# Optimization experiments

Measured on AMD Instinct MI355X. Metric: run time of the kernel, lower is better.

The kernel has to match this reference:

```python
import jax, jax.numpy as jnp
import numpy as np

NUM_CLASSES = 19
EPS_MEAN = 1e-6   # torch: denominator eps in per-class mean
EPS_COS = 1e-8    # torch CosineSimilarity default eps


def _nearest_resize_labels(target, H, W):
    # torch nn.Upsample(mode='nearest'): in_idx = floor(out_idx * in / out)
    th, tw = target.shape[1], target.shape[2]
    ih = (jnp.arange(H) * th) // H
    iw = (jnp.arange(W) * tw) // W
    return target[:, ih][:, :, iw]  # [B,H,W]


def _class_centers(feat, lab):
    # feat: [B,C,H,W]; lab: [B,H,W] int. Single-pass segment mean by class,
    # then scatter means back to pixels whose label is in [0, NUM_CLASSES).
    B, C, H, W = feat.shape
    f = feat.reshape(B, C, H * W)                 # [B,C,N]
    l = lab.reshape(B, H * W)                      # [B,N]
    onehot = jax.nn.one_hot(l, NUM_CLASSES, dtype=feat.dtype)  # [B,N,K]; out-of-range -> all-zero row
    sums = jnp.einsum('bcn,bnk->bck', f, onehot)   # per-class channel sums
    counts = onehot.sum(axis=1)                    # [B,K]
    means = sums / (counts[:, None, :] + EPS_MEAN) # [B,C,K]
    gathered = jnp.einsum('bck,bnk->bcn', means, onehot)  # mean at each valid pixel, 0 elsewhere
    valid = (l >= 0) & (l < NUM_CLASSES)           # [B,N]
    center = jnp.where(valid[:, None, :], gathered, f)
    return center.reshape(B, C, H, W)


def _cosine_dim1(a, b):
    # torch CosineSimilarity(dim=1): dot / (max(||a||,eps) * max(||b||,eps))
    num = (a * b).sum(axis=1)
    na = jnp.sqrt((a * a).sum(axis=1))
    nb = jnp.sqrt((b * b).sum(axis=1))
    return num / (jnp.maximum(na, EPS_COS) * jnp.maximum(nb, EPS_COS))


def setup_inputs() -> dict:
    key = jax.random.key(0)
    k1, k2, k3 = jax.random.split(key, 3)
    B, C, H, W = 8, 512, 64, 64
    preds_S = jax.random.normal(k1, (B, C, H, W), dtype=jnp.float32)
    preds_T = jax.random.normal(k2, (B, C, H, W), dtype=jnp.float32)
    target = jax.random.randint(k3, (B, 512, 512), 0, NUM_CLASSES, dtype=jnp.int64)
    return {"preds_S": preds_S, "preds_T": preds_T, "target": target}


def reference(preds_S, preds_T, target):
    H, W = preds_S.shape[2], preds_S.shape[3]
    lab = _nearest_resize_labels(target, H, W)     # [B,H,W]
    center_S = _class_centers(preds_S, lab)
    center_T = _class_centers(preds_T, lab)
    pcsim_S = _cosine_dim1(preds_S, center_S)      # [B,H,W]
    pcsim_T = _cosine_dim1(preds_T, center_T)
    return jnp.mean((pcsim_S - pcsim_T) ** 2)
```

## Files before the change

### kernel.cpp

```cpp
#include <hip/hip_runtime.h>

#define NCLS   19
#define NB     8
#define NC     512
#define NHW    4096
#define EPSM   1e-6f
#define EPSC   1e-8f

#define OFF_LABELS   0u
#define OFF_COUNTS   131072u
#define OFF_SUMS_S   132096u
#define OFF_SUMS_T   443392u
#define OFF_NORM_S   754688u
#define OFF_NORM_T   755712u
#define OFF_PART     756736u

template<int CTRL>
__device__ __forceinline__ float dpp_add(float x) {
    int y = __builtin_amdgcn_update_dpp(0, __float_as_int(x), CTRL, 0xf, 0xf, false);
    return x + __int_as_float(y);
}
__device__ __forceinline__ float wave64_sum(float x) {
    x = dpp_add<0x111>(x);
    x = dpp_add<0x112>(x);
    x = dpp_add<0x114>(x);
    x = dpp_add<0x118>(x);
    x = dpp_add<0x142>(x);
    x = dpp_add<0x143>(x);
    return x;
}

__global__ __launch_bounds__(256) void k_labels(const int* __restrict__ target,
                                                int* __restrict__ labels,
                                                float* __restrict__ counts) {
    __shared__ int hist[NCLS];
    const int b = blockIdx.x;
    const int t = threadIdx.x;
    if (t < NCLS) hist[t] = 0;
    __syncthreads();
    const int* tb = target + (size_t)b * 512 * 512;
    #pragma unroll
    for (int i = 0; i < 16; ++i) {
        int n = t + i * 256;
        int y = n >> 6, x = n & 63;
        int l = tb[(y * 8) * 512 + x * 8];
        labels[b * NHW + n] = l;
        if (l >= 0 && l < NCLS) atomicAdd(&hist[l], 1);
    }
    __syncthreads();
    if (t < NCLS) counts[b * NCLS + t] = (float)hist[t];
}

__global__ __launch_bounds__(256, 2) void k_sums(const float* __restrict__ fS,
                                                 const float* __restrict__ fT,
                                                 const int* __restrict__ labels,
                                                 float* __restrict__ sumsS,
                                                 float* __restrict__ sumsT) {
    const int t = threadIdx.x;
    const int lane = t & 63;
    const int u = (blockIdx.x << 2) + (t >> 6);
    const int b = u >> 8;
    const int c0 = (u & 255) << 1;
    const size_t base = ((size_t)(b * NC) + c0) * NHW;
    const float4* pS0 = (const float4*)(fS + base);
    const float4* pS1 = (const float4*)(fS + base + NHW);
    const float4* pT0 = (const float4*)(fT + base);
    const float4* pT1 = (const float4*)(fT + base + NHW);
    const int4* lab4 = (const int4*)(labels + b * NHW);

    float aS0[NCLS], aS1[NCLS], aT0[NCLS], aT1[NCLS];
    #pragma unroll
    for (int k = 0; k < NCLS; ++k) { aS0[k] = aS1[k] = aT0[k] = aT1[k] = 0.f; }

    #pragma unroll 2
    for (int i = 0; i < 16; ++i) {
        const int idx = lane + (i << 6);
        const float4 vS0 = pS0[idx];
        const float4 vS1 = pS1[idx];
        const float4 vT0 = pT0[idx];
        const float4 vT1 = pT1[idx];
        const int4 l4 = lab4[idx];
        #pragma unroll
        for (int k = 0; k < NCLS; ++k) {
            const float m0 = (l4.x == k) ? 1.f : 0.f;
            const float m1 = (l4.y == k) ? 1.f : 0.f;
            const float m2 = (l4.z == k) ? 1.f : 0.f;
            const float m3 = (l4.w == k) ? 1.f : 0.f;
            aS0[k] += m0 * vS0.x + m1 * vS0.y + m2 * vS0.z + m3 * vS0.w;
            aS1[k] += m0 * vS1.x + m1 * vS1.y + m2 * vS1.z + m3 * vS1.w;
            aT0[k] += m0 * vT0.x + m1 * vT0.y + m2 * vT0.z + m3 * vT0.w;
            aT1[k] += m0 * vT1.x + m1 * vT1.y + m2 * vT1.z + m3 * vT1.w;
        }
    }
    #pragma unroll
    for (int k = 0; k < NCLS; ++k) {
        aS0[k] = wave64_sum(aS0[k]);
        aS1[k] = wave64_sum(aS1[k]);
        aT0[k] = wave64_sum(aT0[k]);
        aT1[k] = wave64_sum(aT1[k]);
    }
    if (lane == 63) {
        #pragma unroll
        for (int k = 0; k < NCLS; ++k) {
            float2* dS = (float2*)(sumsS + ((size_t)(b * NCLS + k)) * NC + c0);
            float2* dT = (float2*)(sumsT + ((size_t)(b * NCLS + k)) * NC + c0);
            *dS = make_float2(aS0[k], aS1[k]);
            *dT = make_float2(aT0[k], aT1[k]);
        }
    }
}

__global__ __launch_bounds__(64) void k_means(float* __restrict__ sumsS,
                                              float* __restrict__ sumsT,
                                              const float* __restrict__ counts,
                                              float* __restrict__ normS,
                                              float* __restrict__ normT) {
    const int bk = blockIdx.x;
    const int t = threadIdx.x;
    const float inv = 1.f / (counts[bk] + EPSM);
    float* rS = sumsS + (size_t)bk * NC;
    float* rT = sumsT + (size_t)bk * NC;
    float aS = 0.f, aT = 0.f;
    #pragma unroll
    for (int i = 0; i < NC / 64; ++i) {
        float mS = rS[t + i * 64] * inv; rS[t + i * 64] = mS; aS += mS * mS;
        float mT = rT[t + i * 64] * inv; rT[t + i * 64] = mT; aT += mT * mT;
    }
    aS = wave64_sum(aS);
    aT = wave64_sum(aT);
    if (t == 63) { normS[bk] = sqrtf(aS); normT[bk] = sqrtf(aT); }
}

#define CCH 64
__global__ __launch_bounds__(256) void k_dots(const float* __restrict__ fS,
                                              const float* __restrict__ fT,
                                              const float* __restrict__ meansS,
                                              const float* __restrict__ meansT,
                                              const int* __restrict__ labels,
                                              float* __restrict__ part) {
    __shared__ float mS[NCLS * 65];
    __shared__ float mT[NCLS * 65];
    const int blk = blockIdx.x;
    const int chunk = blk & 7;
    const int tile  = (blk >> 3) & 15;
    const int b     = blk >> 7;
    const int t = threadIdx.x;
    const int c0 = chunk * CCH;
    const int n = tile * 256 + t;

    for (int i = t; i < NCLS * CCH; i += 256) {
        const int k = i >> 6, j = i & 63;
        mS[k * 65 + j] = meansS[((size_t)(b * NCLS + k)) * NC + c0 + j];
        mT[k * 65 + j] = meansT[((size_t)(b * NCLS + k)) * NC + c0 + j];
    }
    __syncthreads();

    const int l = labels[b * NHW + n];
    const int lc = (l >= 0 && l < NCLS) ? l : 0;
    const float* pS = fS + ((size_t)(b * NC + c0)) * NHW + n;
    const float* pT = fT + ((size_t)(b * NC + c0)) * NHW + n;
    float dS = 0.f, nS = 0.f, dT = 0.f, nT = 0.f;
    #pragma unroll 8
    for (int ci = 0; ci < CCH; ++ci) {
        const float vS = pS[(size_t)ci * NHW];
        const float vT = pT[(size_t)ci * NHW];
        const float ms = mS[lc * 65 + ci];
        const float mt = mT[lc * 65 + ci];
        dS += vS * ms; nS += vS * vS;
        dT += vT * mt; nT += vT * vT;
    }
    const int p = b * NHW + n;
    part[((size_t)(0 * 8 + chunk)) * (NB * NHW) + p] = dS;
    part[((size_t)(1 * 8 + chunk)) * (NB * NHW) + p] = nS;
    part[((size_t)(2 * 8 + chunk)) * (NB * NHW) + p] = dT;
    part[((size_t)(3 * 8 + chunk)) * (NB * NHW) + p] = nT;
}

__global__ __launch_bounds__(256) void k_final(const float* __restrict__ part,
                                               const int* __restrict__ labels,
                                               const float* __restrict__ normS,
                                               const float* __restrict__ normT,
                                               float* __restrict__ out) {
    __shared__ float red[4];
    const int p = blockIdx.x * 256 + threadIdx.x;
    const int b = p >> 12;
    float dS = 0.f, nS = 0.f, dT = 0.f, nT = 0.f;
    #pragma unroll
    for (int ch = 0; ch < 8; ++ch) {
        dS += part[((size_t)(0 * 8 + ch)) * (NB * NHW) + p];
        nS += part[((size_t)(1 * 8 + ch)) * (NB * NHW) + p];
        dT += part[((size_t)(2 * 8 + ch)) * (NB * NHW) + p];
        nT += part[((size_t)(3 * 8 + ch)) * (NB * NHW) + p];
    }
    const int l = labels[p];
    float val = 0.f;
    if (l >= 0 && l < NCLS) {
        float cS = dS / (fmaxf(sqrtf(nS), EPSC) * fmaxf(normS[b * NCLS + l], EPSC));
        float cT = dT / (fmaxf(sqrtf(nT), EPSC) * fmaxf(normT[b * NCLS + l], EPSC));
        float d = cS - cT;
        val = d * d;
    }
    val = wave64_sum(val);
    if ((threadIdx.x & 63) == 63) red[threadIdx.x >> 6] = val;
    __syncthreads();
    if (threadIdx.x == 0)
        atomicAdd(out, (red[0] + red[1] + red[2] + red[3]) * (1.f / (NB * NHW)));
}

extern "C" void kernel_launch(void* const* d_in, const int* in_sizes, int n_in,
                              void* d_out, int out_size, void* d_ws, size_t ws_size,
                              hipStream_t stream) {
    (void)in_sizes; (void)n_in; (void)out_size; (void)ws_size;
    const float* fS     = (const float*)d_in[0];
    const float* fT     = (const float*)d_in[1];
    const int*   target = (const int*)d_in[2];

    char* ws = (char*)d_ws;
    int*   labels = (int*)  (ws + OFF_LABELS);
    float* counts = (float*)(ws + OFF_COUNTS);
    float* sumsS  = (float*)(ws + OFF_SUMS_S);
    float* sumsT  = (float*)(ws + OFF_SUMS_T);
    float* normS  = (float*)(ws + OFF_NORM_S);
    float* normT  = (float*)(ws + OFF_NORM_T);
    float* part   = (float*)(ws + OFF_PART);

    hipMemsetAsync(d_out, 0, sizeof(float), stream);

    k_labels<<<NB, 256, 0, stream>>>(target, labels, counts);
    k_sums  <<<NB * NC / 8, 256, 0, stream>>>(fS, fT, labels, sumsS, sumsT);
    k_means <<<NB * NCLS, 64, 0, stream>>>(sumsS, sumsT, counts, normS, normT);
    k_dots  <<<NB * 16 * 8, 256, 0, stream>>>(fS, fT, sumsS, sumsT, labels, part);
    k_final <<<NB * NHW / 256, 256, 0, stream>>>(part, labels, normS, normT,
                                                 (float*)d_out);
}
```

Measured before the change: 207.8 us.

## Replace masked per-class register accumulation with LDS atomic scatter-add in k_sums

```diff
diff --git a/kernel.cpp b/kernel.cpp
--- a/kernel.cpp
+++ b/kernel.cpp
@@ -6,6 +6,7 @@
 #define NHW    4096
 #define EPSM   1e-6f
 #define EPSC   1e-8f
+#define GCH    2
 
 #define OFF_LABELS   0u
 #define OFF_COUNTS   131072u
@@ -51,62 +52,51 @@
     if (t < NCLS) counts[b * NCLS + t] = (float)hist[t];
 }
 
-__global__ __launch_bounds__(256, 2) void k_sums(const float* __restrict__ fS,
-                                                 const float* __restrict__ fT,
-                                                 const int* __restrict__ labels,
-                                                 float* __restrict__ sumsS,
-                                                 float* __restrict__ sumsT) {
-    const int t = threadIdx.x;
-    const int lane = t & 63;
-    const int u = (blockIdx.x << 2) + (t >> 6);
-    const int b = u >> 8;
-    const int c0 = (u & 255) << 1;
-    const size_t base = ((size_t)(b * NC) + c0) * NHW;
-    const float4* pS0 = (const float4*)(fS + base);
-    const float4* pS1 = (const float4*)(fS + base + NHW);
-    const float4* pT0 = (const float4*)(fT + base);
-    const float4* pT1 = (const float4*)(fT + base + NHW);
+__global__ __launch_bounds__(256) void k_sums(const float* __restrict__ fS,
+                                              const float* __restrict__ fT,
+                                              const int* __restrict__ labels,
+                                              float* __restrict__ sumsS,
+                                              float* __restrict__ sumsT) {
+    __shared__ float acc[NCLS][5];
+    const int t   = threadIdx.x;
+    const int blk = blockIdx.x;
+    const int b   = blk >> 8;
+    const int cg  = blk & 255;
+    const int c0  = cg * GCH;
+
+    for (int i = t; i < NCLS * 5; i += 256) ((float*)acc)[i] = 0.f;
+    __syncthreads();
+
     const int4* lab4 = (const int4*)(labels + b * NHW);
-
-    float aS0[NCLS], aS1[NCLS], aT0[NCLS], aT1[NCLS];
-    #pragma unroll
-    for (int k = 0; k < NCLS; ++k) { aS0[k] = aS1[k] = aT0[k] = aT1[k] = 0.f; }
-
-    #pragma unroll 2
-    for (int i = 0; i < 16; ++i) {
-        const int idx = lane + (i << 6);
-        const float4 vS0 = pS0[idx];
-        const float4 vS1 = pS1[idx];
-        const float4 vT0 = pT0[idx];
-        const float4 vT1 = pT1[idx];
-        const int4 l4 = lab4[idx];
+    int4 lab[4];
+    #pragma unroll
+    for (int j = 0; j < 4; ++j) lab[j] = lab4[t + 256 * j];
+
+    #pragma unroll
+    for (int ci = 0; ci < GCH; ++ci) {
+        const size_t base = ((size_t)(b * NC) + c0 + ci) * NHW;
+        const float4* pS = (const float4*)(fS + base);
+        const float4* pT = (const float4*)(fT + base);
+        const int sS = ci * 2, sT = ci * 2 + 1;
         #pragma unroll
-        for (int k = 0; k < NCLS; ++k) {
-            const float m0 = (l4.x == k) ? 1.f : 0.f;
-            const float m1 = (l4.y == k) ? 1.f : 0.f;
-            const float m2 = (l4.z == k) ? 1.f : 0.f;
-            const float m3 = (l4.w == k) ? 1.f : 0.f;
-            aS0[k] += m0 * vS0.x + m1 * vS0.y + m2 * vS0.z + m3 * vS0.w;
-            aS1[k] += m0 * vS1.x + m1 * vS1.y + m2 * vS1.z + m3 * vS1.w;
-            aT0[k] += m0 * vT0.x + m1 * vT0.y + m2 * vT0.z + m3 * vT0.w;
-            aT1[k] += m0 * vT1.x + m1 * vT1.y + m2 * vT1.z + m3 * vT1.w;
+        for (int j = 0; j < 4; ++j) {
+            const float4 vS = pS[t + 256 * j];
+            const float4 vT = pT[t + 256 * j];
+            const int4 l = lab[j];
+            if ((unsigned)l.x < NCLS) { atomicAdd(&acc[l.x][sS], vS.x); atomicAdd(&acc[l.x][sT], vT.x); }
+            if ((unsigned)l.y < NCLS) { atomicAdd(&acc[l.y][sS], vS.y); atomicAdd(&acc[l.y][sT], vT.y); }
+            if ((unsigned)l.z < NCLS) { atomicAdd(&acc[l.z][sS], vS.z); atomicAdd(&acc[l.z][sT], vT.z); }
+            if ((unsigned)l.w < NCLS) { atomicAdd(&acc[l.w][sS], vS.w); atomicAdd(&acc[l.w][sT], vT.w); }
         }
     }
-    #pragma unroll
-    for (int k = 0; k < NCLS; ++k) {
-        aS0[k] = wave64_sum(aS0[k]);
-        aS1[k] = wave64_sum(aS1[k]);
-        aT0[k] = wave64_sum(aT0[k]);
-        aT1[k] = wave64_sum(aT1[k]);
-    }
-    if (lane == 63) {
-        #pragma unroll
-        for (int k = 0; k < NCLS; ++k) {
-            float2* dS = (float2*)(sumsS + ((size_t)(b * NCLS + k)) * NC + c0);
-            float2* dT = (float2*)(sumsT + ((size_t)(b * NCLS + k)) * NC + c0);
-            *dS = make_float2(aS0[k], aS1[k]);
-            *dT = make_float2(aT0[k], aT1[k]);
-        }
+    __syncthreads();
+
+    for (int i = t; i < NCLS * GCH * 2; i += 256) {
+        const int k  = i / (GCH * 2);
+        const int s  = i % (GCH * 2);
+        const int ci = s >> 1, ten = s & 1;
+        float* dst = (ten ? sumsT : sumsS) + ((size_t)(b * NCLS + k)) * NC + c0 + ci;
+        *dst = acc[k][s];
     }
 }
 
@@ -227,7 +217,7 @@
     hipMemsetAsync(d_out, 0, sizeof(float), stream);
 
     k_labels<<<NB, 256, 0, stream>>>(target, labels, counts);
-    k_sums  <<<NB * NC / 8, 256, 0, stream>>>(fS, fT, labels, sumsS, sumsT);
+    k_sums  <<<NB * (NC / GCH), 256, 0, stream>>>(fS, fT, labels, sumsS, sumsT);
     k_means <<<NB * NCLS, 64, 0, stream>>>(sumsS, sumsT, counts, normS, normT);
     k_dots  <<<NB * 16 * 8, 256, 0, stream>>>(fS, fT, sumsS, sumsT, labels, part);
     k_final <<<NB * NHW / 256, 256, 0, stream>>>(part, labels, normS, normT,
```

Measured after the change: 325.1 us. +56.5%, slower.
